# Performance work log

Hardware: AMD Instinct MI355X
Metric: run time of the kernel (lower is better)

## Reference

```python
import jax, jax.numpy as jnp
import numpy as np

N = 100000   # nodes
E = 1600000  # edges
IN = 128     # in_dim
HID = 64     # hidden_dim per head
H = 4        # heads
OUT = 2      # out_dim (classes)
HD = HID * H # 256
NEG_SLOPE = 0.2
BN_EPS = 1e-5


def setup_inputs() -> dict:
    key = jax.random.key(0)
    ks = jax.random.split(key, 24)
    rn = lambda k, shp, s=0.05: (jax.random.normal(k, shp, jnp.float32) * s)
    d = {}
    d['x'] = jax.random.normal(ks[0], (N, IN), jnp.float32)
    d['edge_index'] = jax.random.randint(ks[1], (2, E), 0, N, dtype=jnp.int64)
    # layer 0: 128 -> (4,64)
    d['W0'] = rn(ks[2], (IN, HD))
    d['a_src0'] = rn(ks[3], (H, HID), 0.1)
    d['a_dst0'] = rn(ks[4], (H, HID), 0.1)
    d['b0'] = jnp.zeros((HD,), jnp.float32)
    # layer 1: 256 -> (4,64)
    d['W1'] = rn(ks[5], (HD, HD))
    d['a_src1'] = rn(ks[6], (H, HID), 0.1)
    d['a_dst1'] = rn(ks[7], (H, HID), 0.1)
    d['b1'] = jnp.zeros((HD,), jnp.float32)
    # layer 2: 256 -> (1,2), concat=False
    d['W2'] = rn(ks[8], (HD, OUT))
    d['a_src2'] = rn(ks[9], (1, OUT), 0.1)
    d['a_dst2'] = rn(ks[10], (1, OUT), 0.1)
    d['b2'] = jnp.zeros((OUT,), jnp.float32)
    # skip projection for layer 0 (128 != 256)
    d['skipW'] = rn(ks[11], (IN, HD))
    d['skipb'] = jnp.zeros((HD,), jnp.float32)
    # batchnorm affine params
    d['g0'] = jnp.ones((HD,), jnp.float32); d['be0'] = jnp.zeros((HD,), jnp.float32)
    d['g1'] = jnp.ones((HD,), jnp.float32); d['be1'] = jnp.zeros((HD,), jnp.float32)
    d['g2'] = jnp.ones((OUT,), jnp.float32); d['be2'] = jnp.zeros((OUT,), jnp.float32)
    return d


def _gat_conv(x, src, dst, W, a_src, a_dst, b, heads, ch, concat):
    n = x.shape[0]
    h = (x @ W).reshape(n, heads, ch)                 # [N,H,C]
    alpha_src = jnp.sum(h * a_src, axis=-1)           # [N,H]
    alpha_dst = jnp.sum(h * a_dst, axis=-1)           # [N,H]
    e = alpha_src[src] + alpha_dst[dst]               # [E',H]
    e = jax.nn.leaky_relu(e, NEG_SLOPE)
    # segment softmax over incoming edges of each dst node
    m = jax.ops.segment_max(e, dst, num_segments=n)
    e = jnp.exp(e - m[dst])
    s = jax.ops.segment_sum(e, dst, num_segments=n)
    alpha = e / (s[dst] + 1e-16)                      # [E',H]
    out = jax.ops.segment_sum(h[src] * alpha[..., None], dst, num_segments=n)  # [N,H,C]
    out = out.reshape(n, heads * ch) if concat else out.mean(axis=1)
    return out + b


def _bn(x, g, b):
    mu = x.mean(axis=0)
    v = x.var(axis=0)  # biased, matches torch BN training normalization
    return g * (x - mu) * jax.lax.rsqrt(v + BN_EPS) + b


def reference(x, edge_index, W0, a_src0, a_dst0, b0, W1, a_src1, a_dst1, b1,
              W2, a_src2, a_dst2, b2, skipW, skipb, g0, be0, g1, be1, g2, be2):
    n = x.shape[0]
    loop = jnp.arange(n, dtype=edge_index.dtype)
    src = jnp.concatenate([edge_index[0], loop])  # self-loops (PyG default)
    dst = jnp.concatenate([edge_index[1], loop])

    residual = x
    # layer 0
    h = _gat_conv(x, src, dst, W0, a_src0, a_dst0, b0, H, HID, True)
    h = _bn(h, g0, be0)
    h = h + (residual @ skipW + skipb)
    residual = h
    h = jax.nn.elu(h)
    # layer 1
    h = _gat_conv(h, src, dst, W1, a_src1, a_dst1, b1, H, HID, True)
    h = _bn(h, g1, be1)
    h = h + residual  # Identity skip
    h = jax.nn.elu(h)
    # layer 2 (heads=1, concat=False)
    h = _gat_conv(h, src, dst, W2, a_src2, a_dst2, b2, 1, OUT, False)
    h = _bn(h, g2, be2)
    return h
```

## Files before the change

### kernel.cpp

```cpp
#include <hip/hip_runtime.h>
#include <cstdint>
#include <cstddef>

#define KN 100000
#define KE 1600000
#define KE2 (KE + KN)
#define KIN 128
#define KHD 256
#define KH 4

#define BSH 7
#define NBUK ((KN + 127) >> 7)
#define BCAP 2560
#define ACHUNK 8192

#define LRELU(x) ((x) > 0.f ? (x) : 0.2f * (x))

typedef unsigned short bfu;
typedef short bf16x8 __attribute__((ext_vector_type(8)));
typedef unsigned short u16x8 __attribute__((ext_vector_type(8)));
typedef float f32x4 __attribute__((ext_vector_type(4)));

__device__ __forceinline__ float bf2f(bfu u) {
    union { unsigned int i; float f; } c; c.i = ((unsigned int)u) << 16; return c.f;
}
__device__ __forceinline__ bfu f2bf(float f) {
    union { float f; unsigned int i; } c; c.f = f;
    unsigned int r = c.i + 0x7FFFu + ((c.i >> 16) & 1u);
    return (bfu)(r >> 16);
}
__device__ __forceinline__ float eluf(float x) { return x > 0.f ? x : expm1f(x); }

__global__ __launch_bounds__(256) void k_binA(const int* __restrict__ ei,
                                              int* __restrict__ gcur,
                                              uint2* __restrict__ stg) {
    __shared__ int cnt[NBUK];
    __shared__ int base[NBUK];
    int t = threadIdx.x;
    for (int i = t; i < NBUK; i += 256) cnt[i] = 0;
    __syncthreads();
    int e0 = blockIdx.x * ACHUNK;
    int rank[ACHUNK / 256];
#pragma unroll
    for (int i = 0; i < ACHUNK / 256; ++i) {
        int e = e0 + i * 256 + t;
        rank[i] = 0;
        if (e < KE2) {
            int d = (e < KE) ? ei[KE + e] : (e - KE);
            rank[i] = atomicAdd(&cnt[d >> BSH], 1);
        }
    }
    __syncthreads();
    for (int b = t; b < NBUK; b += 256) {
        int c = cnt[b];
        base[b] = c ? atomicAdd(&gcur[b], c) : 0;
    }
    __syncthreads();
#pragma unroll
    for (int i = 0; i < ACHUNK / 256; ++i) {
        int e = e0 + i * 256 + t;
        if (e < KE2) {
            int d = (e < KE) ? ei[KE + e] : (e - KE);
            int s = (e < KE) ? ei[e] : (e - KE);
            int b = d >> BSH;
            int pos = base[b] + rank[i];
            if (pos < BCAP) stg[(size_t)b * BCAP + pos] = make_uint2((unsigned)s, (unsigned)d);
        }
    }
}

__global__ __launch_bounds__(1024) void k_scanB(const int* __restrict__ gcur,
                                                int* __restrict__ gbase,
                                                int* __restrict__ rowptr) {
    __shared__ int s[1024];
    int t = threadIdx.x;
    int v = (t < NBUK) ? min(gcur[t], BCAP) : 0;
    s[t] = v;
    __syncthreads();
    for (int o = 1; o < 1024; o <<= 1) {
        int add = (t >= o) ? s[t - o] : 0;
        __syncthreads();
        s[t] += add;
        __syncthreads();
    }
    if (t < NBUK) gbase[t] = s[t] - v;
    if (t == 0) rowptr[KN] = KE2;
}

__global__ __launch_bounds__(256) void k_binB(const int* __restrict__ gcur,
                                              const int* __restrict__ gbase,
                                              const uint2* __restrict__ stg,
                                              int* __restrict__ rowptr,
                                              int* __restrict__ csrc) {
    __shared__ int lcnt[128];
    __shared__ int lcur[128];
    __shared__ int ss[128];
    __shared__ int loff[128];
    int b = blockIdx.x, t = threadIdx.x;
    if (t < 128) { lcnt[t] = 0; lcur[t] = 0; }
    __syncthreads();
    int n = min(gcur[b], BCAP);
    int node0 = b << BSH;
    const uint2* sp = stg + (size_t)b * BCAP;
    for (int i = t; i < n; i += 256) {
        int d = (int)sp[i].y;
        atomicAdd(&lcnt[d - node0], 1);
    }
    __syncthreads();
    int v = (t < 128) ? lcnt[t] : 0;
    if (t < 128) ss[t] = v;
    __syncthreads();
    for (int o = 1; o < 128; o <<= 1) {
        int add = (t < 128 && t >= o) ? ss[t - o] : 0;
        __syncthreads();
        if (t < 128) ss[t] += add;
        __syncthreads();
    }
    int gb = gbase[b];
    if (t < 128) {
        loff[t] = ss[t] - v;
        int node = node0 + t;
        if (node < KN) rowptr[node] = gb + ss[t] - v;
    }
    __syncthreads();
    for (int i = t; i < n; i += 256) {
        uint2 r = sp[i];
        int li = (int)r.y - node0;
        int rank = atomicAdd(&lcur[li], 1);
        csrc[gb + loff[li] + rank] = (int)r.x;
    }
}

__global__ void k_cvt_w(const float* __restrict__ W, bfu* __restrict__ Wt, int K) {
    int t = blockIdx.x * 256 + threadIdx.x;
    if (t >= K * 256) return;
    int n = t & 255;
    int k = t >> 8;
    Wt[(size_t)n * K + k] = f2bf(W[(size_t)k * 256 + n]);
}

template<int AMODE, int ALPHA>
__global__ __launch_bounds__(256) void k_mgemm(const void* __restrict__ Ap,
                                               const bfu* __restrict__ Wt,
                                               const float* __restrict__ bias,
                                               bfu* __restrict__ Cout, int M, int K,
                                               const float* __restrict__ avs,
                                               const float* __restrict__ avd,
                                               float* __restrict__ as_out,
                                               float* __restrict__ ad_out) {
    __shared__ bfu As[128 * 40];
    __shared__ bfu Bs[128 * 40];
    int t = threadIdx.x;
    int row0 = blockIdx.x * 128;
    int col0 = blockIdx.y * 128;
    int srow = t >> 1;
    int shalf = t & 1;
    int l = t & 63;
    int w = t >> 6;
    int wr = w >> 1, wc = w & 1;
    int lg = l >> 4, lm = l & 15;

    f32x4 acc[4][4] = {};

    for (int kk = 0; kk < K; kk += 32) {
        {
            int garow = row0 + srow;
            bfu abuf[16];
            if (garow < M) {
                if (AMODE == 0) {
                    const float* ap = (const float*)Ap + (size_t)garow * K + kk + shalf * 16;
#pragma unroll
                    for (int i = 0; i < 4; ++i) {
                        float4 v = ((const float4*)ap)[i];
                        abuf[i * 4 + 0] = f2bf(v.x); abuf[i * 4 + 1] = f2bf(v.y);
                        abuf[i * 4 + 2] = f2bf(v.z); abuf[i * 4 + 3] = f2bf(v.w);
                    }
                } else {
                    const bfu* ap = (const bfu*)Ap + (size_t)garow * K + kk + shalf * 16;
                    u16x8 u0 = *(const u16x8*)ap;
                    u16x8 u1 = *(const u16x8*)(ap + 8);
#pragma unroll
                    for (int i = 0; i < 8; ++i) abuf[i] = f2bf(eluf(bf2f(u0[i])));
#pragma unroll
                    for (int i = 0; i < 8; ++i) abuf[8 + i] = f2bf(eluf(bf2f(u1[i])));
                }
            } else {
#pragma unroll
                for (int i = 0; i < 16; ++i) abuf[i] = 0;
            }
            *(u16x8*)(&As[srow * 40 + shalf * 16]) = *(const u16x8*)(&abuf[0]);
            *(u16x8*)(&As[srow * 40 + shalf * 16 + 8]) = *(const u16x8*)(&abuf[8]);
        }
        {
            const bfu* bp = Wt + (size_t)(col0 + srow) * K + kk + shalf * 16;
            *(u16x8*)(&Bs[srow * 40 + shalf * 16]) = *(const u16x8*)bp;
            *(u16x8*)(&Bs[srow * 40 + shalf * 16 + 8]) = *(const u16x8*)(bp + 8);
        }
        __syncthreads();
        {
            int a_base = (wr * 64 + lm) * 40 + lg * 8;
            int b_base = (wc * 64 + lm) * 40 + lg * 8;
            bf16x8 af[4], bf_[4];
#pragma unroll
            for (int m = 0; m < 4; ++m) af[m] = *(const bf16x8*)(&As[a_base + m * 16 * 40]);
#pragma unroll
            for (int n = 0; n < 4; ++n) bf_[n] = *(const bf16x8*)(&Bs[b_base + n * 16 * 40]);
#pragma unroll
            for (int m = 0; m < 4; ++m)
#pragma unroll
                for (int n = 0; n < 4; ++n)
                    acc[m][n] = __builtin_amdgcn_mfma_f32_16x16x32_bf16(af[m], bf_[n], acc[m][n], 0, 0, 0);
        }
        __syncthreads();
    }

    if (ALPHA) {
        int head = (blockIdx.y << 1) + wc;
        const float* ah_s = avs + head * 64;
        const float* ah_d = avd + head * 64;
        float wsv[4], wdv[4];
#pragma unroll
        for (int n = 0; n < 4; ++n) {
            wsv[n] = ah_s[n * 16 + lm];
            wdv[n] = ah_d[n * 16 + lm];
        }
#pragma unroll
        for (int m = 0; m < 4; ++m) {
#pragma unroll
            for (int r = 0; r < 4; ++r) {
                float ps = 0.f, pd = 0.f;
#pragma unroll
                for (int n = 0; n < 4; ++n) {
                    float v = acc[m][n][r];
                    ps += v * wsv[n];
                    pd += v * wdv[n];
                }
#pragma unroll
                for (int off = 1; off < 16; off <<= 1) {
                    ps += __shfl_xor(ps, off, 16);
                    pd += __shfl_xor(pd, off, 16);
                }
                int rrow = row0 + wr * 64 + m * 16 + lg * 4 + r;
                if (lm == 0 && rrow < M) {
                    as_out[rrow * 4 + head] = ps;
                    ad_out[rrow * 4 + head] = pd;
                }
            }
        }
    }

    float bv[4];
#pragma unroll
    for (int n = 0; n < 4; ++n)
        bv[n] = bias ? bias[col0 + wc * 64 + n * 16 + lm] : 0.f;
#pragma unroll
    for (int m = 0; m < 4; ++m) {
#pragma unroll
        for (int r = 0; r < 4; ++r) {
            int rrow = row0 + wr * 64 + m * 16 + lg * 4 + r;
            if (rrow < M) {
                size_t base = (size_t)rrow * 256 + col0 + wc * 64 + lm;
#pragma unroll
                for (int n = 0; n < 4; ++n)
                    Cout[base + n * 16] = f2bf(acc[m][n][r] + bv[n]);
            }
        }
    }
}

__global__ __launch_bounds__(256) void k_gat_agg(const bfu* __restrict__ h,
                                                 const int* __restrict__ rowptr,
                                                 const int* __restrict__ csrc,
                                                 const float* __restrict__ asrc,
                                                 const float* __restrict__ adst,
                                                 const float* __restrict__ bias,
                                                 bfu* __restrict__ outb) {
    int wave = threadIdx.x >> 6, lane = threadIdx.x & 63;
    int node = blockIdx.x * 4 + wave;
    if (node >= KN) return;
    int p0 = rowptr[node], p1 = rowptr[node + 1];
    int head = lane >> 4;
    int c0 = lane << 2;
    float adh = adst[node * 4 + head];

    float sum = 0.f, a0 = 0.f, a1 = 0.f, a2 = 0.f, a3 = 0.f;
    int p = p0;
    for (; p + 3 < p1; p += 4) {
        int s0 = csrc[p], s1 = csrc[p + 1], s2 = csrc[p + 2], s3 = csrc[p + 3];
        float e0 = asrc[s0 * 4 + head] + adh; e0 = LRELU(e0);
        float e1 = asrc[s1 * 4 + head] + adh; e1 = LRELU(e1);
        float e2 = asrc[s2 * 4 + head] + adh; e2 = LRELU(e2);
        float e3 = asrc[s3 * 4 + head] + adh; e3 = LRELU(e3);
        float w0 = __expf(e0), w1 = __expf(e1), w2 = __expf(e2), w3 = __expf(e3);
        ushort4 u0 = *(const ushort4*)(h + (size_t)s0 * 256 + c0);
        ushort4 u1 = *(const ushort4*)(h + (size_t)s1 * 256 + c0);
        ushort4 u2 = *(const ushort4*)(h + (size_t)s2 * 256 + c0);
        ushort4 u3 = *(const ushort4*)(h + (size_t)s3 * 256 + c0);
        a0 += bf2f(u0.x) * w0 + bf2f(u1.x) * w1 + bf2f(u2.x) * w2 + bf2f(u3.x) * w3;
        a1 += bf2f(u0.y) * w0 + bf2f(u1.y) * w1 + bf2f(u2.y) * w2 + bf2f(u3.y) * w3;
        a2 += bf2f(u0.z) * w0 + bf2f(u1.z) * w1 + bf2f(u2.z) * w2 + bf2f(u3.z) * w3;
        a3 += bf2f(u0.w) * w0 + bf2f(u1.w) * w1 + bf2f(u2.w) * w2 + bf2f(u3.w) * w3;
        sum += (w0 + w1) + (w2 + w3);
    }
    for (; p < p1; ++p) {
        int s = csrc[p];
        float e = asrc[s * 4 + head] + adh; e = LRELU(e);
        float w = __expf(e);
        ushort4 u = *(const ushort4*)(h + (size_t)s * 256 + c0);
        a0 += bf2f(u.x) * w; a1 += bf2f(u.y) * w;
        a2 += bf2f(u.z) * w; a3 += bf2f(u.w) * w;
        sum += w;
    }
    float inv = 1.f / (sum + 1e-16f);
    float4 bv = *(const float4*)(bias + c0);
    ushort4 o;
    o.x = f2bf(a0 * inv + bv.x);
    o.y = f2bf(a1 * inv + bv.y);
    o.z = f2bf(a2 * inv + bv.z);
    o.w = f2bf(a3 * inv + bv.w);
    *(ushort4*)(outb + (size_t)node * 256 + c0) = o;
}

__global__ __launch_bounds__(256) void k_bn_stats(const bfu* __restrict__ xx,
                                                  float* __restrict__ sums,
                                                  float* __restrict__ sumsq) {
    int t = threadIdx.x;
    float s = 0.f, q = 0.f;
    for (int row = blockIdx.x; row < KN; row += gridDim.x) {
        float v = bf2f(xx[(size_t)row * 256 + t]);
        s += v; q += v * v;
    }
    atomicAdd(&sums[t], s);
    atomicAdd(&sumsq[t], q);
}

__global__ void k_bn_params(const float* __restrict__ sums, const float* __restrict__ sumsq,
                            const float* __restrict__ g, const float* __restrict__ be,
                            float* __restrict__ scaleC, float* __restrict__ shiftC) {
    int c = threadIdx.x;
    float mean = sums[c] / (float)KN;
    float var = sumsq[c] / (float)KN - mean * mean;
    float inv = rsqrtf(var + 1e-5f);
    float sc = g[c] * inv;
    scaleC[c] = sc;
    shiftC[c] = be[c] - mean * sc;
}

__global__ __launch_bounds__(256) void k_finalize_skip(bfu* __restrict__ P,
                                                       const bfu* __restrict__ skipQ,
                                                       const float* __restrict__ scaleC,
                                                       const float* __restrict__ shiftC) {
    size_t i = (size_t)blockIdx.x * 256 + threadIdx.x;
    int c = threadIdx.x;
    float r = bf2f(P[i]) * scaleC[c] + shiftC[c] + bf2f(skipQ[i]);
    P[i] = f2bf(r);
}

__global__ __launch_bounds__(256) void k_finalize_add(const bfu* __restrict__ Q,
                                                      bfu* __restrict__ P,
                                                      const float* __restrict__ scaleC,
                                                      const float* __restrict__ shiftC) {
    size_t i = (size_t)blockIdx.x * 256 + threadIdx.x;
    int c = threadIdx.x;
    float r = bf2f(Q[i]) * scaleC[c] + shiftC[c] + bf2f(P[i]);
    P[i] = f2bf(eluf(r));
}

__global__ __launch_bounds__(256) void k_gemm2(const bfu* __restrict__ xx,
                                               const float* __restrict__ W,
                                               const float* __restrict__ as2,
                                               const float* __restrict__ ad2,
                                               float* __restrict__ h2,
                                               float* __restrict__ asrc,
                                               float* __restrict__ adst) {
    int lane = threadIdx.x & 63;
    int node = blockIdx.x * 4 + (threadIdx.x >> 6);
    if (node >= KN) return;
    float a0 = 0.f, a1 = 0.f;
    for (int k = lane; k < 256; k += 64) {
        float v = bf2f(xx[(size_t)node * 256 + k]);
        a0 += v * W[2 * k];
        a1 += v * W[2 * k + 1];
    }
    for (int o = 32; o > 0; o >>= 1) { a0 += __shfl_down(a0, o); a1 += __shfl_down(a1, o); }
    if (lane == 0) {
        h2[2 * node] = a0; h2[2 * node + 1] = a1;
        asrc[node] = a0 * as2[0] + a1 * as2[1];
        adst[node] = a0 * ad2[0] + a1 * ad2[1];
    }
}

__global__ void k_gat_agg2(const float* __restrict__ h2, const int* __restrict__ rowptr,
                           const int* __restrict__ csrc, const float* __restrict__ asrc,
                           const float* __restrict__ adst, const float* __restrict__ b2,
                           float* __restrict__ agg2) {
    int node = blockIdx.x * blockDim.x + threadIdx.x;
    if (node >= KN) return;
    int p0 = rowptr[node], p1 = rowptr[node + 1];
    float ad = adst[node];
    float sum = 0.f, acc0 = 0.f, acc1 = 0.f;
    int p = p0;
    for (; p + 1 < p1; p += 2) {
        int s0 = csrc[p], s1 = csrc[p + 1];
        float e0 = asrc[s0] + ad; e0 = LRELU(e0);
        float e1 = asrc[s1] + ad; e1 = LRELU(e1);
        float w0 = __expf(e0), w1 = __expf(e1);
        float2 v0 = *(const float2*)(h2 + 2 * s0);
        float2 v1 = *(const float2*)(h2 + 2 * s1);
        acc0 += w0 * v0.x + w1 * v1.x;
        acc1 += w0 * v0.y + w1 * v1.y;
        sum += w0 + w1;
    }
    if (p < p1) {
        int s = csrc[p];
        float e = asrc[s] + ad; e = LRELU(e);
        float w = __expf(e);
        float2 v = *(const float2*)(h2 + 2 * s);
        acc0 += w * v.x; acc1 += w * v.y;
        sum += w;
    }
    float inv = 1.f / (sum + 1e-16f);
    agg2[2 * node] = acc0 * inv + b2[0];
    agg2[2 * node + 1] = acc1 * inv + b2[1];
}

__global__ __launch_bounds__(256) void k_bn_stats2(const float* __restrict__ xx,
                                                   float* __restrict__ st) {
    int t = threadIdx.x;
    float s0 = 0, q0 = 0, s1 = 0, q1 = 0;
    for (int i = blockIdx.x * 256 + t; i < KN; i += gridDim.x * 256) {
        float v0 = xx[2 * i], v1 = xx[2 * i + 1];
        s0 += v0; q0 += v0 * v0; s1 += v1; q1 += v1 * v1;
    }
    for (int o = 32; o > 0; o >>= 1) {
        s0 += __shfl_down(s0, o); q0 += __shfl_down(q0, o);
        s1 += __shfl_down(s1, o); q1 += __shfl_down(q1, o);
    }
    __shared__ float red[4][4];
    int lane = t & 63, wv = t >> 6;
    if (lane == 0) { red[wv][0] = s0; red[wv][1] = q0; red[wv][2] = s1; red[wv][3] = q1; }
    __syncthreads();
    if (t == 0) {
        float a = 0, b = 0, c = 0, d = 0;
        for (int w = 0; w < 4; ++w) { a += red[w][0]; b += red[w][1]; c += red[w][2]; d += red[w][3]; }
        atomicAdd(&st[0], a); atomicAdd(&st[1], b); atomicAdd(&st[2], c); atomicAdd(&st[3], d);
    }
}

__global__ void k_finalize2(const float* __restrict__ agg2, const float* __restrict__ st,
                            const float* __restrict__ g, const float* __restrict__ be,
                            float* __restrict__ outp) {
    int i = blockIdx.x * blockDim.x + threadIdx.x;
    if (i >= 2 * KN) return;
    int c = i & 1;
    float mean = st[c * 2] / (float)KN;
    float var = st[c * 2 + 1] / (float)KN - mean * mean;
    float inv = rsqrtf(var + 1e-5f);
    outp[i] = (agg2[i] - mean) * g[c] * inv + be[c];
}

extern "C" void kernel_launch(void* const* d_in, const int* in_sizes, int n_in,
                              void* d_out, int out_size, void* d_ws, size_t ws_size,
                              hipStream_t stream) {
    (void)in_sizes; (void)n_in; (void)out_size; (void)ws_size;
    const float* x     = (const float*)d_in[0];
    const int*   ei    = (const int*)d_in[1];
    const float* W0    = (const float*)d_in[2];
    const float* as0   = (const float*)d_in[3];
    const float* ad0   = (const float*)d_in[4];
    const float* b0    = (const float*)d_in[5];
    const float* W1    = (const float*)d_in[6];
    const float* as1   = (const float*)d_in[7];
    const float* ad1   = (const float*)d_in[8];
    const float* b1    = (const float*)d_in[9];
    const float* W2    = (const float*)d_in[10];
    const float* as2   = (const float*)d_in[11];
    const float* ad2   = (const float*)d_in[12];
    const float* b2    = (const float*)d_in[13];
    const float* skipW = (const float*)d_in[14];
    const float* skipb = (const float*)d_in[15];
    const float* g0    = (const float*)d_in[16];
    const float* be0   = (const float*)d_in[17];
    const float* g1    = (const float*)d_in[18];
    const float* be1   = (const float*)d_in[19];
    const float* g2    = (const float*)d_in[20];
    const float* be2   = (const float*)d_in[21];
    float* outp = (float*)d_out;

    char* ws = (char*)d_ws;
    size_t off = 0;
    auto alloc = [&](size_t bytes) -> void* {
        void* p = ws + off;
        off += (bytes + 255) & ~(size_t)255;
        return p;
    };
    bfu* hbf = (bfu*)alloc((size_t)KN * KHD * 2);
    bfu* P   = (bfu*)alloc((size_t)KN * KHD * 2);
    bfu* Q   = (bfu*)alloc((size_t)KN * KHD * 2);
    int* rowptr   = (int*)alloc((size_t)(KN + 1) * 4);
    int* csrc     = (int*)alloc((size_t)KE2 * 4);
    int* gcur     = (int*)alloc((size_t)NBUK * 4);
    int* gbase    = (int*)alloc((size_t)NBUK * 4);
    uint2* stg    = (uint2*)alloc((size_t)NBUK * BCAP * 8);
    float* asrcb  = (float*)alloc((size_t)KN * KH * 4);
    float* adstb  = (float*)alloc((size_t)KN * KH * 4);
    float* sums   = (float*)alloc(256 * 4);
    float* sumsq  = (float*)alloc(256 * 4);
    float* scaleC = (float*)alloc(256 * 4);
    float* shiftC = (float*)alloc(256 * 4);
    float* h2     = (float*)alloc((size_t)KN * 2 * 4);
    float* agg2   = (float*)alloc((size_t)KN * 2 * 4);
    float* st2    = (float*)alloc(256);
    bfu* W0t      = (bfu*)alloc((size_t)256 * KIN * 2);
    bfu* W1t      = (bfu*)alloc((size_t)256 * KHD * 2);
    bfu* Wst      = (bfu*)alloc((size_t)256 * KIN * 2);

    k_cvt_w<<<KIN, 256, 0, stream>>>(W0, W0t, KIN);
    k_cvt_w<<<KHD, 256, 0, stream>>>(W1, W1t, KHD);
    k_cvt_w<<<KIN, 256, 0, stream>>>(skipW, Wst, KIN);

    hipMemsetAsync(gcur, 0, (size_t)NBUK * 4, stream);
    k_binA<<<(KE2 + ACHUNK - 1) / ACHUNK, 256, 0, stream>>>(ei, gcur, stg);
    k_scanB<<<1, 1024, 0, stream>>>(gcur, gbase, rowptr);
    k_binB<<<NBUK, 256, 0, stream>>>(gcur, gbase, stg, rowptr, csrc);

    dim3 mg((KN + 127) / 128, 2);
    int ngrid = (KN + 255) / 256;

    k_mgemm<0, 1><<<mg, 256, 0, stream>>>(x, W0t, nullptr, hbf, KN, KIN,
                                          as0, ad0, asrcb, adstb);
    k_mgemm<0, 0><<<mg, 256, 0, stream>>>(x, Wst, skipb, Q, KN, KIN,
                                          nullptr, nullptr, nullptr, nullptr);
    k_gat_agg<<<(KN + 3) / 4, 256, 0, stream>>>(hbf, rowptr, csrc, asrcb, adstb, b0, P);
    hipMemsetAsync(sums, 0, 256 * 4, stream);
    hipMemsetAsync(sumsq, 0, 256 * 4, stream);
    k_bn_stats<<<1024, 256, 0, stream>>>(P, sums, sumsq);
    k_bn_params<<<1, 256, 0, stream>>>(sums, sumsq, g0, be0, scaleC, shiftC);
    k_finalize_skip<<<KN, 256, 0, stream>>>(P, Q, scaleC, shiftC);

    k_mgemm<2, 1><<<mg, 256, 0, stream>>>(P, W1t, nullptr, hbf, KN, KHD,
                                          as1, ad1, asrcb, adstb);
    k_gat_agg<<<(KN + 3) / 4, 256, 0, stream>>>(hbf, rowptr, csrc, asrcb, adstb, b1, Q);
    hipMemsetAsync(sums, 0, 256 * 4, stream);
    hipMemsetAsync(sumsq, 0, 256 * 4, stream);
    k_bn_stats<<<1024, 256, 0, stream>>>(Q, sums, sumsq);
    k_bn_params<<<1, 256, 0, stream>>>(sums, sumsq, g1, be1, scaleC, shiftC);
    k_finalize_add<<<KN, 256, 0, stream>>>(Q, P, scaleC, shiftC);

    k_gemm2<<<(KN + 3) / 4, 256, 0, stream>>>(P, W2, as2, ad2, h2, asrcb, adstb);
    k_gat_agg2<<<ngrid, 256, 0, stream>>>(h2, rowptr, csrc, asrcb, adstb, b2, agg2);
    hipMemsetAsync(st2, 0, 4 * 4, stream);
    k_bn_stats2<<<256, 256, 0, stream>>>(agg2, st2);
    k_finalize2<<<(2 * KN + 255) / 256, 256, 0, stream>>>(agg2, st2, g2, be2, outp);
}
```

Baseline: 760.7 us.

## Fuse layer-0 GEMMs, vectorize gather/finalize kernels, grid-stride final projection

Concatenates W0 and skipW into one weight matrix so a single GEMM launch with four column tiles produces both the layer-0 features and the skip projection, reading x once per tile set. The GAT aggregation loop now aligns to 4 edges, loads source indices as int4, and issues 8 row gathers before computing weights, to get more memory loads in flight. The finalize kernels process 8 bf16 elements per thread with vector loads. The final 256→2 projection uses a grid-stride loop with each lane holding 4 weights. These add code size and register pressure in the aggregation kernel in exchange for fewer launches and fewer narrow memory operations.

```diff
diff --git a/kernel.cpp b/kernel.cpp
--- a/kernel.cpp
+++ b/kernel.cpp
@@ -139,15 +139,16 @@
     Wt[(size_t)n * K + k] = f2bf(W[(size_t)k * 256 + n]);
 }
 
-template<int AMODE, int ALPHA>
-__global__ __launch_bounds__(256) void k_mgemm(const void* __restrict__ Ap,
-                                               const bfu* __restrict__ Wt,
-                                               const float* __restrict__ bias,
-                                               bfu* __restrict__ Cout, int M, int K,
-                                               const float* __restrict__ avs,
-                                               const float* __restrict__ avd,
-                                               float* __restrict__ as_out,
-                                               float* __restrict__ ad_out) {
+__global__ __launch_bounds__(256) void k_mgemm_dual(const float* __restrict__ Ap,
+                                                    const bfu* __restrict__ Wcat,
+                                                    const float* __restrict__ skipb,
+                                                    bfu* __restrict__ hout,
+                                                    bfu* __restrict__ sout, int M,
+                                                    const float* __restrict__ avs,
+                                                    const float* __restrict__ avd,
+                                                    float* __restrict__ as_out,
+                                                    float* __restrict__ ad_out) {
+    const int K = KIN;
     __shared__ bfu As[128 * 40];
     __shared__ bfu Bs[128 * 40];
     int t = threadIdx.x;
@@ -167,22 +168,12 @@
             int garow = row0 + srow;
             bfu abuf[16];
             if (garow < M) {
-                if (AMODE == 0) {
-                    const float* ap = (const float*)Ap + (size_t)garow * K + kk + shalf * 16;
-#pragma unroll
-                    for (int i = 0; i < 4; ++i) {
-                        float4 v = ((const float4*)ap)[i];
-                        abuf[i * 4 + 0] = f2bf(v.x); abuf[i * 4 + 1] = f2bf(v.y);
-                        abuf[i * 4 + 2] = f2bf(v.z); abuf[i * 4 + 3] = f2bf(v.w);
-                    }
-                } else {
-                    const bfu* ap = (const bfu*)Ap + (size_t)garow * K + kk + shalf * 16;
-                    u16x8 u0 = *(const u16x8*)ap;
-                    u16x8 u1 = *(const u16x8*)(ap + 8);
-#pragma unroll
-                    for (int i = 0; i < 8; ++i) abuf[i] = f2bf(eluf(bf2f(u0[i])));
-#pragma unroll
-                    for (int i = 0; i < 8; ++i) abuf[8 + i] = f2bf(eluf(bf2f(u1[i])));
+                const float* ap = Ap + (size_t)garow * K + kk + shalf * 16;
+#pragma unroll
+                for (int i = 0; i < 4; ++i) {
+                    float4 v = ((const float4*)ap)[i];
+                    abuf[i * 4 + 0] = f2bf(v.x); abuf[i * 4 + 1] = f2bf(v.y);
+                    abuf[i * 4 + 2] = f2bf(v.z); abuf[i * 4 + 3] = f2bf(v.w);
                 }
             } else {
 #pragma unroll
@@ -192,7 +183,7 @@
             *(u16x8*)(&As[srow * 40 + shalf * 16 + 8]) = *(const u16x8*)(&abuf[8]);
         }
         {
-            const bfu* bp = Wt + (size_t)(col0 + srow) * K + kk + shalf * 16;
+            const bfu* bp = Wcat + (size_t)(col0 + srow) * K + kk + shalf * 16;
             *(u16x8*)(&Bs[srow * 40 + shalf * 16]) = *(const u16x8*)bp;
             *(u16x8*)(&Bs[srow * 40 + shalf * 16 + 8]) = *(const u16x8*)(bp + 8);
         }
@@ -214,7 +205,8 @@
         __syncthreads();
     }
 
-    if (ALPHA) {
+    bool isH = (blockIdx.y < 2);
+    if (isH) {
         int head = (blockIdx.y << 1) + wc;
         const float* ah_s = avs + head * 64;
         const float* ah_d = avd + head * 64;
@@ -249,10 +241,126 @@
         }
     }
 
+    bfu* outp = isH ? hout : sout;
+    int ocol = (isH ? col0 : col0 - 256) + wc * 64 + lm;
     float bv[4];
 #pragma unroll
     for (int n = 0; n < 4; ++n)
-        bv[n] = bias ? bias[col0 + wc * 64 + n * 16 + lm] : 0.f;
+        bv[n] = isH ? 0.f : skipb[ocol + n * 16];
+#pragma unroll
+    for (int m = 0; m < 4; ++m) {
+#pragma unroll
+        for (int r = 0; r < 4; ++r) {
+            int rrow = row0 + wr * 64 + m * 16 + lg * 4 + r;
+            if (rrow < M) {
+                size_t base = (size_t)rrow * 256 + ocol;
+#pragma unroll
+                for (int n = 0; n < 4; ++n)
+                    outp[base + n * 16] = f2bf(acc[m][n][r] + bv[n]);
+            }
+        }
+    }
+}
+
+__global__ __launch_bounds__(256) void k_mgemm1(const bfu* __restrict__ Ap,
+                                                const bfu* __restrict__ Wt,
+                                                bfu* __restrict__ Cout, int M,
+                                                const float* __restrict__ avs,
+                                                const float* __restrict__ avd,
+                                                float* __restrict__ as_out,
+                                                float* __restrict__ ad_out) {
+    const int K = KHD;
+    __shared__ bfu As[128 * 40];
+    __shared__ bfu Bs[128 * 40];
+    int t = threadIdx.x;
+    int row0 = blockIdx.x * 128;
+    int col0 = blockIdx.y * 128;
+    int srow = t >> 1;
+    int shalf = t & 1;
+    int l = t & 63;
+    int w = t >> 6;
+    int wr = w >> 1, wc = w & 1;
+    int lg = l >> 4, lm = l & 15;
+
+    f32x4 acc[4][4] = {};
+
+    for (int kk = 0; kk < K; kk += 32) {
+        {
+            int garow = row0 + srow;
+            bfu abuf[16];
+            if (garow < M) {
+                const bfu* ap = Ap + (size_t)garow * K + kk + shalf * 16;
+                u16x8 u0 = *(const u16x8*)ap;
+                u16x8 u1 = *(const u16x8*)(ap + 8);
+#pragma unroll
+                for (int i = 0; i < 8; ++i) abuf[i] = f2bf(eluf(bf2f(u0[i])));
+#pragma unroll
+                for (int i = 0; i < 8; ++i) abuf[8 + i] = f2bf(eluf(bf2f(u1[i])));
+            } else {
+#pragma unroll
+                for (int i = 0; i < 16; ++i) abuf[i] = 0;
+            }
+            *(u16x8*)(&As[srow * 40 + shalf * 16]) = *(const u16x8*)(&abuf[0]);
+            *(u16x8*)(&As[srow * 40 + shalf * 16 + 8]) = *(const u16x8*)(&abuf[8]);
+        }
+        {
+            const bfu* bp = Wt + (size_t)(col0 + srow) * K + kk + shalf * 16;
+            *(u16x8*)(&Bs[srow * 40 + shalf * 16]) = *(const u16x8*)bp;
+            *(u16x8*)(&Bs[srow * 40 + shalf * 16 + 8]) = *(const u16x8*)(bp + 8);
+        }
+        __syncthreads();
+        {
+            int a_base = (wr * 64 + lm) * 40 + lg * 8;
+            int b_base = (wc * 64 + lm) * 40 + lg * 8;
+            bf16x8 af[4], bf_[4];
+#pragma unroll
+            for (int m = 0; m < 4; ++m) af[m] = *(const bf16x8*)(&As[a_base + m * 16 * 40]);
+#pragma unroll
+            for (int n = 0; n < 4; ++n) bf_[n] = *(const bf16x8*)(&Bs[b_base + n * 16 * 40]);
+#pragma unroll
+            for (int m = 0; m < 4; ++m)
+#pragma unroll
+                for (int n = 0; n < 4; ++n)
+                    acc[m][n] = __builtin_amdgcn_mfma_f32_16x16x32_bf16(af[m], bf_[n], acc[m][n], 0, 0, 0);
+        }
+        __syncthreads();
+    }
+
+    {
+        int head = (blockIdx.y << 1) + wc;
+        const float* ah_s = avs + head * 64;
+        const float* ah_d = avd + head * 64;
+        float wsv[4], wdv[4];
+#pragma unroll
+        for (int n = 0; n < 4; ++n) {
+            wsv[n] = ah_s[n * 16 + lm];
+            wdv[n] = ah_d[n * 16 + lm];
+        }
+#pragma unroll
+        for (int m = 0; m < 4; ++m) {
+#pragma unroll
+            for (int r = 0; r < 4; ++r) {
+                float ps = 0.f, pd = 0.f;
+#pragma unroll
+                for (int n = 0; n < 4; ++n) {
+                    float v = acc[m][n][r];
+                    ps += v * wsv[n];
+                    pd += v * wdv[n];
+                }
+#pragma unroll
+                for (int off = 1; off < 16; off <<= 1) {
+                    ps += __shfl_xor(ps, off, 16);
+                    pd += __shfl_xor(pd, off, 16);
+                }
+                int rrow = row0 + wr * 64 + m * 16 + lg * 4 + r;
+                if (lm == 0 && rrow < M) {
+                    as_out[rrow * 4 + head] = ps;
+                    ad_out[rrow * 4 + head] = pd;
+                }
+            }
+        }
+    }
+
 #pragma unroll
     for (int m = 0; m < 4; ++m) {
 #pragma unroll
@@ -262,7 +370,7 @@
                 size_t base = (size_t)rrow * 256 + col0 + wc * 64 + lm;
 #pragma unroll
                 for (int n = 0; n < 4; ++n)
-                    Cout[base + n * 16] = f2bf(acc[m][n][r] + bv[n]);
+                    Cout[base + n * 16] = f2bf(acc[m][n][r] + 0.f);
             }
         }
     }
@@ -285,22 +393,54 @@
 
     float sum = 0.f, a0 = 0.f, a1 = 0.f, a2 = 0.f, a3 = 0.f;
     int p = p0;
+    while (p < p1 && (p & 3)) {
+        int s = csrc[p];
+        float e = asrc[s * 4 + head] + adh; e = LRELU(e);
+        float w = __expf(e);
+        ushort4 u = *(const ushort4*)(h + (size_t)s * 256 + c0);
+        a0 += bf2f(u.x) * w; a1 += bf2f(u.y) * w;
+        a2 += bf2f(u.z) * w; a3 += bf2f(u.w) * w;
+        sum += w;
+        ++p;
+    }
+    for (; p + 7 < p1; p += 8) {
+        int4 ca = *(const int4*)(csrc + p);
+        int4 cb = *(const int4*)(csrc + p + 4);
+        int sx[8] = {ca.x, ca.y, ca.z, ca.w, cb.x, cb.y, cb.z, cb.w};
+        ushort4 u[8];
+#pragma unroll
+        for (int j = 0; j < 8; ++j)
+            u[j] = *(const ushort4*)(h + (size_t)sx[j] * 256 + c0);
+        float wv[8];
+#pragma unroll
+        for (int j = 0; j < 8; ++j) {
+            float e = asrc[sx[j] * 4 + head] + adh; e = LRELU(e);
+            wv[j] = __expf(e);
+        }
+#pragma unroll
+        for (int j = 0; j < 8; ++j) {
+            a0 += bf2f(u[j].x) * wv[j];
+            a1 += bf2f(u[j].y) * wv[j];
+            a2 += bf2f(u[j].z) * wv[j];
+            a3 += bf2f(u[j].w) * wv[j];
+            sum += wv[j];
+        }
+    }
     for (; p + 3 < p1; p += 4) {
-        int s0 = csrc[p], s1 = csrc[p + 1], s2 = csrc[p + 2], s3 = csrc[p + 3];
-        float e0 = asrc[s0 * 4 + head] + adh; e0 = LRELU(e0);
-        float e1 = asrc[s1 * 4 + head] + adh; e1 = LRELU(e1);
-        float e2 = asrc[s2 * 4 + head] + adh; e2 = LRELU(e2);
-        float e3 = asrc[s3 * 4 + head] + adh; e3 = LRELU(e3);
-        float w0 = __expf(e0), w1 = __expf(e1), w2 = __expf(e2), w3 = __expf(e3);
-        ushort4 u0 = *(const ushort4*)(h + (size_t)s0 * 256 + c0);
-        ushort4 u1 = *(const ushort4*)(h + (size_t)s1 * 256 + c0);
-        ushort4 u2 = *(const ushort4*)(h + (size_t)s2 * 256 + c0);
-        ushort4 u3 = *(const ushort4*)(h + (size_t)s3 * 256 + c0);
-        a0 += bf2f(u0.x) * w0 + bf2f(u1.x) * w1 + bf2f(u2.x) * w2 + bf2f(u3.x) * w3;
-        a1 += bf2f(u0.y) * w0 + bf2f(u1.y) * w1 + bf2f(u2.y) * w2 + bf2f(u3.y) * w3;
-        a2 += bf2f(u0.z) * w0 + bf2f(u1.z) * w1 + bf2f(u2.z) * w2 + bf2f(u3.z) * w3;
-        a3 += bf2f(u0.w) * w0 + bf2f(u1.w) * w1 + bf2f(u2.w) * w2 + bf2f(u3.w) * w3;
-        sum += (w0 + w1) + (w2 + w3);
+        int4 ca = *(const int4*)(csrc + p);
+        int sx[4] = {ca.x, ca.y, ca.z, ca.w};
+        ushort4 u[4];
+#pragma unroll
+        for (int j = 0; j < 4; ++j)
+            u[j] = *(const ushort4*)(h + (size_t)sx[j] * 256 + c0);
+#pragma unroll
+        for (int j = 0; j < 4; ++j) {
+            float e = asrc[sx[j] * 4 + head] + adh; e = LRELU(e);
+            float w = __expf(e);
+            a0 += bf2f(u[j].x) * w; a1 += bf2f(u[j].y) * w;
+            a2 += bf2f(u[j].z) * w; a3 += bf2f(u[j].w) * w;
+            sum += w;
+        }
     }
     for (; p < p1; ++p) {
         int s = csrc[p];
@@ -350,20 +490,46 @@
                                                        const bfu* __restrict__ skipQ,
                                                        const float* __restrict__ scaleC,
                                                        const float* __restrict__ shiftC) {
-    size_t i = (size_t)blockIdx.x * 256 + threadIdx.x;
-    int c = threadIdx.x;
-    float r = bf2f(P[i]) * scaleC[c] + shiftC[c] + bf2f(skipQ[i]);
-    P[i] = f2bf(r);
+    size_t i = ((size_t)blockIdx.x * 256 + threadIdx.x) * 8;
+    int c0 = (int)(i & 255);
+    u16x8 pv = *(const u16x8*)(P + i);
+    u16x8 qv = *(const u16x8*)(skipQ + i);
+    float4 s0 = *(const float4*)(scaleC + c0);
+    float4 s1 = *(const float4*)(scaleC + c0 + 4);
+    float4 h0 = *(const float4*)(shiftC + c0);
+    float4 h1 = *(const float4*)(shiftC + c0 + 4);
+    float sc[8] = {s0.x, s0.y, s0.z, s0.w, s1.x, s1.y, s1.z, s1.w};
+    float sh[8] = {h0.x, h0.y, h0.z, h0.w, h1.x, h1.y, h1.z, h1.w};
+    u16x8 o;
+#pragma unroll
+    for (int j = 0; j < 8; ++j) {
+        float r = bf2f(pv[j]) * sc[j] + sh[j] + bf2f(qv[j]);
+        o[j] = f2bf(r);
+    }
+    *(u16x8*)(P + i) = o;
 }
 
 __global__ __launch_bounds__(256) void k_finalize_add(const bfu* __restrict__ Q,
                                                       bfu* __restrict__ P,
                                                       const float* __restrict__ scaleC,
                                                       const float* __restrict__ shiftC) {
-    size_t i = (size_t)blockIdx.x * 256 + threadIdx.x;
-    int c = threadIdx.x;
-    float r = bf2f(Q[i]) * scaleC[c] + shiftC[c] + bf2f(P[i]);
-    P[i] = f2bf(eluf(r));
+    size_t i = ((size_t)blockIdx.x * 256 + threadIdx.x) * 8;
+    int c0 = (int)(i & 255);
+    u16x8 qv = *(const u16x8*)(Q + i);
+    u16x8 pv = *(const u16x8*)(P + i);
+    float4 s0 = *(const float4*)(scaleC + c0);
+    float4 s1 = *(const float4*)(scaleC + c0 + 4);
+    float4 h0 = *(const float4*)(shiftC + c0);
+    float4 h1 = *(const float4*)(shiftC + c0 + 4);
+    float sc[8] = {s0.x, s0.y, s0.z, s0.w, s1.x, s1.y, s1.z, s1.w};
+    float sh[8] = {h0.x, h0.y, h0.z, h0.w, h1.x, h1.y, h1.z, h1.w};
+    u16x8 o;
+#pragma unroll
+    for (int j = 0; j < 8; ++j) {
+        float r = bf2f(qv[j]) * sc[j] + sh[j] + bf2f(pv[j]);
+        o[j] = f2bf(eluf(r));
+    }
+    *(u16x8*)(P + i) = o;
 }
 
 __global__ __launch_bounds__(256) void k_gemm2(const bfu* __restrict__ xx,
@@ -374,19 +540,28 @@
                                                float* __restrict__ asrc,
                                                float* __restrict__ adst) {
     int lane = threadIdx.x & 63;
-    int node = blockIdx.x * 4 + (threadIdx.x >> 6);
-    if (node >= KN) return;
-    float a0 = 0.f, a1 = 0.f;
-    for (int k = lane; k < 256; k += 64) {
-        float v = bf2f(xx[(size_t)node * 256 + k]);
-        a0 += v * W[2 * k];
-        a1 += v * W[2 * k + 1];
-    }
-    for (int o = 32; o > 0; o >>= 1) { a0 += __shfl_down(a0, o); a1 += __shfl_down(a1, o); }
-    if (lane == 0) {
-        h2[2 * node] = a0; h2[2 * node + 1] = a1;
-        asrc[node] = a0 * as2[0] + a1 * as2[1];
-        adst[node] = a0 * ad2[0] + a1 * ad2[1];
+    int wid = blockIdx.x * 4 + (threadIdx.x >> 6);
+    int c = lane * 4;
+    float2 w0 = *(const float2*)(W + 2 * (c + 0));
+    float2 w1 = *(const float2*)(W + 2 * (c + 1));
+    float2 w2 = *(const float2*)(W + 2 * (c + 2));
+    float2 w3 = *(const float2*)(W + 2 * (c + 3));
+    float s0 = as2[0], s1 = as2[1], d0 = ad2[0], d1 = ad2[1];
+    int nwaves = gridDim.x * 4;
+    for (int node = wid; node < KN; node += nwaves) {
+        ushort4 u = *(const ushort4*)(xx + (size_t)node * 256 + c);
+        float v0 = bf2f(u.x), v1 = bf2f(u.y), v2 = bf2f(u.z), v3 = bf2f(u.w);
+        float a0 = v0 * w0.x + v1 * w1.x + v2 * w2.x + v3 * w3.x;
+        float a1 = v0 * w0.y + v1 * w1.y + v2 * w2.y + v3 * w3.y;
+        for (int o = 32; o > 0; o >>= 1) {
+            a0 += __shfl_down(a0, o);
+            a1 += __shfl_down(a1, o);
+        }
+        if (lane == 0) {
+            h2[2 * node] = a0; h2[2 * node + 1] = a1;
+            asrc[node] = a0 * s0 + a1 * s1;
+            adst[node] = a0 * d0 + a1 * d1;
+        }
     }
 }
 
@@ -511,43 +686,40 @@
     float* h2     = (float*)alloc((size_t)KN * 2 * 4);
     float* agg2   = (float*)alloc((size_t)KN * 2 * 4);
     float* st2    = (float*)alloc(256);
-    bfu* W0t      = (bfu*)alloc((size_t)256 * KIN * 2);
+    bfu* Wcat     = (bfu*)alloc((size_t)512 * KIN * 2);
     bfu* W1t      = (bfu*)alloc((size_t)256 * KHD * 2);
-    bfu* Wst      = (bfu*)alloc((size_t)256 * KIN * 2);
-
-    k_cvt_w<<<KIN, 256, 0, stream>>>(W0, W0t, KIN);
+
+    k_cvt_w<<<KIN, 256, 0, stream>>>(W0, Wcat, KIN);
+    k_cvt_w<<<KIN, 256, 0, stream>>>(skipW, Wcat + (size_t)256 * KIN, KIN);
     k_cvt_w<<<KHD, 256, 0, stream>>>(W1, W1t, KHD);
-    k_cvt_w<<<KIN, 256, 0, stream>>>(skipW, Wst, KIN);
 
     hipMemsetAsync(gcur, 0, (size_t)NBUK * 4, stream);
     k_binA<<<(KE2 + ACHUNK - 1) / ACHUNK, 256, 0, stream>>>(ei, gcur, stg);
     k_scanB<<<1, 1024, 0, stream>>>(gcur, gbase, rowptr);
     k_binB<<<NBUK, 256, 0, stream>>>(gcur, gbase, stg, rowptr, csrc);
 
-    dim3 mg((KN + 127) / 128, 2);
     int ngrid = (KN + 255) / 256;
 
-    k_mgemm<0, 1><<<mg, 256, 0, stream>>>(x, W0t, nullptr, hbf, KN, KIN,
+    dim3 mgd((KN + 127) / 128, 4);
+    k_mgemm_dual<<<mgd, 256, 0, stream>>>(x, Wcat, skipb, hbf, Q, KN,
                                           as0, ad0, asrcb, adstb);
-    k_mgemm<0, 0><<<mg, 256, 0, stream>>>(x, Wst, skipb, Q, KN, KIN,
-                                          nullptr, nullptr, nullptr, nullptr);
     k_gat_agg<<<(KN + 3) / 4, 256, 0, stream>>>(hbf, rowptr, csrc, asrcb, adstb, b0, P);
     hipMemsetAsync(sums, 0, 256 * 4, stream);
     hipMemsetAsync(sumsq, 0, 256 * 4, stream);
     k_bn_stats<<<1024, 256, 0, stream>>>(P, sums, sumsq);
     k_bn_params<<<1, 256, 0, stream>>>(sums, sumsq, g0, be0, scaleC, shiftC);
-    k_finalize_skip<<<KN, 256, 0, stream>>>(P, Q, scaleC, shiftC);
-
-    k_mgemm<2, 1><<<mg, 256, 0, stream>>>(P, W1t, nullptr, hbf, KN, KHD,
-                                          as1, ad1, asrcb, adstb);
+    k_finalize_skip<<<KN / 8, 256, 0, stream>>>(P, Q, scaleC, shiftC);
+
+    dim3 mg((KN + 127) / 128, 2);
+    k_mgemm1<<<mg, 256, 0, stream>>>(P, W1t, hbf, KN, as1, ad1, asrcb, adstb);
     k_gat_agg<<<(KN + 3) / 4, 256, 0, stream>>>(hbf, rowptr, csrc, asrcb, adstb, b1, Q);
     hipMemsetAsync(sums, 0, 256 * 4, stream);
     hipMemsetAsync(sumsq, 0, 256 * 4, stream);
     k_bn_stats<<<1024, 256, 0, stream>>>(Q, sums, sumsq);
     k_bn_params<<<1, 256, 0, stream>>>(sums, sumsq, g1, be1, scaleC, shiftC);
-    k_finalize_add<<<KN, 256, 0, stream>>>(Q, P, scaleC, shiftC);
-
-    k_gemm2<<<(KN + 3) / 4, 256, 0, stream>>>(P, W2, as2, ad2, h2, asrcb, adstb);
+    k_finalize_add<<<KN / 8, 256, 0, stream>>>(Q, P, scaleC, shiftC);
+
+    k_gemm2<<<1024, 256, 0, stream>>>(P, W2, as2, ad2, h2, asrcb, adstb);
     k_gat_agg2<<<ngrid, 256, 0, stream>>>(h2, rowptr, csrc, asrcb, adstb, b2, agg2);
     hipMemsetAsync(st2, 0, 4 * 4, stream);
     k_bn_stats2<<<256, 256, 0, stream>>>(agg2, st2);
```

Result: faster. 720.7 us (-5.3%).
